# Kernel optimization log

Measured on AMD Instinct MI355X. Metric: run time of the kernel, lower is better.

## Reference

```python
import jax, jax.numpy as jnp
import numpy as np

HIDDEN = 2048
NUM_HEADS = 16
HEAD_DIM = HIDDEN // NUM_HEADS
SCALE = 1.0 / np.sqrt(HEAD_DIM).astype(np.float32)
BATCH, SEQ = 2, 2048


def setup_inputs() -> dict:
    key = jax.random.key(0)
    ks = jax.random.split(key, 9)
    std = 0.02
    inp = {
        'hidden_states': jax.random.normal(ks[0], (BATCH, SEQ, HIDDEN), jnp.float32),
        'attention_mask': jnp.zeros((BATCH, 1, 1, SEQ), jnp.float32),
        'Wq': jax.random.normal(ks[1], (HIDDEN, HIDDEN), jnp.float32) * std,
        'bq': jnp.zeros((HIDDEN,), jnp.float32),
        'Wk': jax.random.normal(ks[2], (HIDDEN, HIDDEN), jnp.float32) * std,
        'bk': jnp.zeros((HIDDEN,), jnp.float32),
        'Wv': jax.random.normal(ks[3], (HIDDEN, HIDDEN), jnp.float32) * std,
        'bv': jnp.zeros((HIDDEN,), jnp.float32),
        'Wo': jax.random.normal(ks[4], (HIDDEN, HIDDEN), jnp.float32) * std,
        'bo': jnp.zeros((HIDDEN,), jnp.float32),
    }
    return inp


def _split_heads(x):
    b, s, _ = x.shape
    return x.reshape(b, s, NUM_HEADS, HEAD_DIM).transpose(0, 2, 1, 3)  # [b,h,s,d]


def reference(hidden_states, attention_mask, Wq, bq, Wk, bk, Wv, bv, Wo, bo):
    # Linear layers (torch convention: y = x @ W.T + b)
    q = _split_heads(hidden_states @ Wq.T + bq)
    k = _split_heads(hidden_states @ Wk.T + bk)
    v = _split_heads(hidden_states @ Wv.T + bv)
    scores = jnp.einsum('bhqd,bhkd->bhqk', q, k) * SCALE
    scores = scores + attention_mask
    weights = jax.nn.softmax(scores, axis=-1)  # dropout is identity in eval
    ctx = jnp.einsum('bhqk,bhkd->bhqd', weights, v)
    b, h, s, d = ctx.shape
    ctx = ctx.transpose(0, 2, 1, 3).reshape(b, s, HIDDEN)
    return ctx @ Wo.T + bo
```

## Files before the change

kernel.cpp:

```cpp
#include <hip/hip_runtime.h>

typedef __bf16 bf16_t;
typedef bf16_t bf16x8 __attribute__((ext_vector_type(8)));
typedef float f32x4 __attribute__((ext_vector_type(4)));

#define HIDDEN 2048
#define SEQ 2048
#define BATCH 2
#define NHEADS 16
#define HDIM 128
#define MTOT (BATCH*SEQ)
#define SCALE 0.088388347648318447f
#define C1EXP2 0.12753102158508967f
#define LOG2E  1.4426950408889634f

__device__ __forceinline__ float dev_exp2(float x) { return __builtin_amdgcn_exp2f(x); }

typedef __attribute__((address_space(1))) const void gvoid_t;
typedef __attribute__((address_space(3))) void svoid_t;
__device__ __forceinline__ void async_copy16(const bf16_t* g, bf16_t* l) {
  __builtin_amdgcn_global_load_lds((gvoid_t*)g, (svoid_t*)l, 16, 0, 0);
}

__global__ void cvt_all(const float* __restrict__ x,  const float* __restrict__ wq,
                        const float* __restrict__ wk, const float* __restrict__ wv,
                        const float* __restrict__ wo,
                        bf16_t* __restrict__ xb, bf16_t* __restrict__ wqkb,
                        bf16_t* __restrict__ wvb, bf16_t* __restrict__ wob) {
  const size_t HH = (size_t)HIDDEN * HIDDEN;
  const float* src; bf16_t* dst;
  switch (blockIdx.y) {
    case 0:  src = x;        dst = xb;        break;
    case 1:  src = x + HH;   dst = xb + HH;   break;
    case 2:  src = wq;       dst = wqkb;      break;
    case 3:  src = wk;       dst = wqkb + HH; break;
    case 4:  src = wv;       dst = wvb;       break;
    default: src = wo;       dst = wob;       break;
  }
  int i = blockIdx.x * 256 + threadIdx.x;
  float4 v = reinterpret_cast<const float4*>(src)[i];
  union { bf16_t h[4]; uint2 u; } t;
  t.h[0] = (bf16_t)v.x; t.h[1] = (bf16_t)v.y; t.h[2] = (bf16_t)v.z; t.h[3] = (bf16_t)v.w;
  reinterpret_cast<uint2*>(dst)[i] = t.u;
}

__global__ void pack_bias2(const float* __restrict__ a, const float* __restrict__ b2,
                           float* __restrict__ out) {
  int i = blockIdx.x * 256 + threadIdx.x;
  out[i] = (i < HIDDEN) ? a[i] : b2[i - HIDDEN];
}

template<bool OUT_BF16, bool ROW_BIAS>
__global__ __launch_bounds__(256, 3)
void gemm_bt(const bf16_t* __restrict__ A, const bf16_t* __restrict__ Bt,
             const float* __restrict__ bias, void* __restrict__ Yv,
             int M, int N, int K, int ldY) {
  __shared__ __align__(16) bf16_t As[128 * 32];
  __shared__ __align__(16) bf16_t Bs[128 * 32];
  const int tid  = threadIdx.x;
  const int lane = tid & 63;
  const int wv   = tid >> 6;
  const int wr   = wv >> 1, wc = wv & 1;
  const int lr   = lane & 15, quad = lane >> 4;
  const int n0   = blockIdx.x * 128;
  const int m0   = blockIdx.y * 128;

  f32x4 acc[4][4] = {};

  const int srow = wv * 16 + (lane >> 2);
  const int scol = (lane & 3) * 8;
  const bf16_t* gA = A  + (size_t)(m0 + srow) * K + scol;
  const bf16_t* gB = Bt + (size_t)(n0 + srow) * K + scol;
  bf16_t* lA = &As[wv * 16 * 32];
  bf16_t* lB = &Bs[wv * 16 * 32];
  const size_t step64 = (size_t)64 * K;

  for (int kt = 0; kt < K; kt += 32) {
    __syncthreads();
    async_copy16(gA,          lA);
    async_copy16(gA + step64, lA + 64 * 32);
    async_copy16(gB,          lB);
    async_copy16(gB + step64, lB + 64 * 32);
    gA += 32; gB += 32;
    __syncthreads();
    bf16x8 af[4], bfr[4];
#pragma unroll
    for (int mi = 0; mi < 4; ++mi)
      af[mi] = *(const bf16x8*)&As[(wr * 64 + mi * 16 + lr) * 32 + quad * 8];
#pragma unroll
    for (int ni = 0; ni < 4; ++ni)
      bfr[ni] = *(const bf16x8*)&Bs[(wc * 64 + ni * 16 + lr) * 32 + quad * 8];
#pragma unroll
    for (int mi = 0; mi < 4; ++mi)
#pragma unroll
      for (int ni = 0; ni < 4; ++ni)
        acc[mi][ni] = __builtin_amdgcn_mfma_f32_16x16x32_bf16(af[mi], bfr[ni], acc[mi][ni], 0, 0, 0);
  }

  float bcol[4];
  if (!ROW_BIAS) {
#pragma unroll
    for (int ni = 0; ni < 4; ++ni) bcol[ni] = bias[n0 + wc * 64 + ni * 16 + lr];
  }
#pragma unroll
  for (int mi = 0; mi < 4; ++mi) {
#pragma unroll
    for (int r = 0; r < 4; ++r) {
      int row = m0 + wr * 64 + mi * 16 + quad * 4 + r;
      float brow = ROW_BIAS ? bias[row] : 0.0f;
      size_t base = (size_t)row * ldY + n0 + wc * 64;
#pragma unroll
      for (int ni = 0; ni < 4; ++ni) {
        float y = acc[mi][ni][r] + (ROW_BIAS ? brow : bcol[ni]);
        int col = ni * 16 + lr;
        if (OUT_BF16) ((bf16_t*)Yv)[base + col] = (bf16_t)y;
        else          ((float*)Yv)[base + col]  = y;
      }
    }
  }
}

#define BQ 128
#define BKV 64
#define LDQK 4096

__global__ __launch_bounds__(256, 2)
void attn_kernel(const bf16_t* __restrict__ QK, const bf16_t* __restrict__ Vt,
                 const float* __restrict__ mask, bf16_t* __restrict__ O) {
  __shared__ __align__(16) bf16_t Ks[2][BKV * 128];
  __shared__ __align__(16) bf16_t Vs[HDIM * BKV];
  __shared__ __align__(16) bf16_t Ps[BQ * BKV];
  __shared__ __align__(16) float  Msk[SEQ];

  const int tid  = threadIdx.x;
  const int lane = tid & 63;
  const int wv   = tid >> 6;
  const int lr   = lane & 15, quad = lane >> 4;
  const int q0   = blockIdx.x * BQ;
  const int bh   = blockIdx.y;
  const int b    = bh >> 4, h = bh & 15;

  const bf16_t* Qg = QK + (size_t)(b * SEQ + q0) * LDQK + h * HDIM;
  const bf16_t* Kg = QK + (size_t)(b * SEQ) * LDQK + HIDDEN + h * HDIM;
  const bf16_t* Vg = Vt + (size_t)(h * HDIM) * MTOT + b * SEQ;
  const float*  mb = mask + b * SEQ;

  bf16x8 qf[2][4];
#pragma unroll
  for (int mi = 0; mi < 2; ++mi)
#pragma unroll
    for (int dk = 0; dk < 4; ++dk)
      qf[mi][dk] = *(const bf16x8*)(Qg + (size_t)(wv * 32 + mi * 16 + lr) * LDQK + dk * 32 + quad * 8);

  for (int i = tid; i < SEQ / 4; i += 256) {
    float4 mv = reinterpret_cast<const float4*>(mb)[i];
    Msk[i * 4 + 0] = mv.x * LOG2E;
    Msk[i * 4 + 1] = mv.y * LOG2E;
    Msk[i * 4 + 2] = mv.z * LOG2E;
    Msk[i * 4 + 3] = mv.w * LOG2E;
  }

  const int kcs = lane & 15;
  const int vcs = lane & 7;
  const bf16_t* kgp[4]; const bf16_t* vgp[4];
  int lKo[4], lVo[4];
#pragma unroll
  for (int i = 0; i < 4; ++i) {
    int kr = wv * 16 + i * 4 + (lane >> 4);
    kgp[i] = Kg + (size_t)kr * LDQK + ((kcs ^ (kr & 15)) * 8);
    lKo[i] = (wv * 16 + i * 4) * 128;
    int vr = wv * 32 + i * 8 + (lane >> 3);
    vgp[i] = Vg + (size_t)vr * MTOT + ((vcs ^ (vr & 7)) * 8);
    lVo[i] = (wv * 32 + i * 8) * 64;
  }

  asm volatile("s_waitcnt vmcnt(0)" ::: "memory");
#pragma unroll
  for (int i = 0; i < 4; ++i) async_copy16(kgp[i], &Ks[0][lKo[i]]);
  asm volatile("s_waitcnt lgkmcnt(0)" ::: "memory");
  __builtin_amdgcn_s_barrier();

  float l_st[2][4] = {};
  f32x4 oacc[2][8] = {};

  for (int kt = 0; kt < SEQ; kt += BKV) {
    const int cur = (kt >> 6) & 1;
    const bf16_t* Kc = &Ks[cur][0];

    asm volatile("s_waitcnt lgkmcnt(0)" ::: "memory");
    __builtin_amdgcn_s_barrier();
#pragma unroll
    for (int i = 0; i < 4; ++i) async_copy16(vgp[i] + kt, &Vs[lVo[i]]);
    if (kt + BKV < SEQ) {
#pragma unroll
      for (int i = 0; i < 4; ++i)
        async_copy16(kgp[i] + (size_t)(kt + BKV) * LDQK, &Ks[cur ^ 1][lKo[i]]);
      asm volatile("s_waitcnt vmcnt(8)" ::: "memory");
    } else {
      asm volatile("s_waitcnt vmcnt(4)" ::: "memory");
    }
    __builtin_amdgcn_s_barrier();
    __builtin_amdgcn_sched_barrier(0);

    float mk[4];
#pragma unroll
    for (int ni = 0; ni < 4; ++ni) mk[ni] = Msk[kt + ni * 16 + lr];

    f32x4 sacc[2][4] = {};
#pragma unroll
    for (int dk = 0; dk < 4; ++dk) {
      bf16x8 kf[4];
#pragma unroll
      for (int ni = 0; ni < 4; ++ni)
        kf[ni] = *(const bf16x8*)&Kc[(ni * 16 + lr) * 128 + (((dk * 4 + quad) ^ lr) * 8)];
#pragma unroll
      for (int mi = 0; mi < 2; ++mi)
#pragma unroll
        for (int ni = 0; ni < 4; ++ni)
          sacc[mi][ni] = __builtin_amdgcn_mfma_f32_16x16x32_bf16(qf[mi][dk], kf[ni], sacc[mi][ni], 0, 0, 0);
    }

#pragma unroll
    for (int mi = 0; mi < 2; ++mi) {
#pragma unroll
      for (int r = 0; r < 4; ++r) {
        float p0 = dev_exp2(fmaf(sacc[mi][0][r], C1EXP2, mk[0]));
        float p1 = dev_exp2(fmaf(sacc[mi][1][r], C1EXP2, mk[1]));
        float p2 = dev_exp2(fmaf(sacc[mi][2][r], C1EXP2, mk[2]));
        float p3 = dev_exp2(fmaf(sacc[mi][3][r], C1EXP2, mk[3]));
        int pr = wv * 32 + mi * 16 + quad * 4 + r;
        int key = pr & 7;
        Ps[pr * BKV + (((0 + (lr >> 3)) ^ key) * 8) + (lr & 7)] = (bf16_t)p0;
        Ps[pr * BKV + (((2 + (lr >> 3)) ^ key) * 8) + (lr & 7)] = (bf16_t)p1;
        Ps[pr * BKV + (((4 + (lr >> 3)) ^ key) * 8) + (lr & 7)] = (bf16_t)p2;
        Ps[pr * BKV + (((6 + (lr >> 3)) ^ key) * 8) + (lr & 7)] = (bf16_t)p3;
        l_st[mi][r] += (p0 + p1) + (p2 + p3);
      }
    }

    if (kt + BKV < SEQ) {
      asm volatile("s_waitcnt vmcnt(4)" ::: "memory");
    } else {
      asm volatile("s_waitcnt vmcnt(0)" ::: "memory");
    }
    __builtin_amdgcn_s_barrier();
    __builtin_amdgcn_sched_barrier(0);

#pragma unroll
    for (int ki = 0; ki < 2; ++ki) {
      bf16x8 pf[2];
#pragma unroll
      for (int mi = 0; mi < 2; ++mi)
        pf[mi] = *(const bf16x8*)&Ps[(wv * 32 + mi * 16 + lr) * BKV + (((ki * 4 + quad) ^ (lr & 7)) * 8)];
#pragma unroll
      for (int di = 0; di < 8; ++di) {
        bf16x8 vf = *(const bf16x8*)&Vs[(di * 16 + lr) * BKV + (((ki * 4 + quad) ^ (lr & 7)) * 8)];
#pragma unroll
        for (int mi = 0; mi < 2; ++mi)
          oacc[mi][di] = __builtin_amdgcn_mfma_f32_16x16x32_bf16(pf[mi], vf, oacc[mi][di], 0, 0, 0);
      }
    }
  }

  bf16_t* Ob = O + (size_t)(b * SEQ + q0) * HIDDEN + h * HDIM;
#pragma unroll
  for (int mi = 0; mi < 2; ++mi) {
#pragma unroll
    for (int r = 0; r < 4; ++r) {
      float s = l_st[mi][r];
      s += __shfl_xor(s, 1);
      s += __shfl_xor(s, 2);
      s += __shfl_xor(s, 4);
      s += __shfl_xor(s, 8);
      float inv = 1.0f / s;
      size_t rowoff = (size_t)(wv * 32 + mi * 16 + quad * 4 + r) * HIDDEN;
#pragma unroll
      for (int di = 0; di < 8; ++di)
        Ob[rowoff + di * 16 + lr] = (bf16_t)(oacc[mi][di][r] * inv);
    }
  }
}

extern "C" void kernel_launch(void* const* d_in, const int* in_sizes, int n_in,
                              void* d_out, int out_size, void* d_ws, size_t ws_size,
                              hipStream_t stream) {
  const float* x   = (const float*)d_in[0];
  const float* msk = (const float*)d_in[1];
  const float* Wq  = (const float*)d_in[2];
  const float* bq  = (const float*)d_in[3];
  const float* Wk  = (const float*)d_in[4];
  const float* bk  = (const float*)d_in[5];
  const float* Wv  = (const float*)d_in[6];
  const float* bv  = (const float*)d_in[7];
  const float* Wo  = (const float*)d_in[8];
  const float* bo  = (const float*)d_in[9];
  float* out = (float*)d_out;

  bf16_t* Xb   = (bf16_t*)d_ws;
  bf16_t* Wqkb = Xb   + (size_t)MTOT * HIDDEN;
  bf16_t* Wvb  = Wqkb + (size_t)2 * HIDDEN * HIDDEN;
  bf16_t* Wob  = Wvb  + (size_t)HIDDEN * HIDDEN;
  bf16_t* QKo  = Wob  + (size_t)HIDDEN * HIDDEN;
  bf16_t* Vto  = QKo  + (size_t)MTOT * 2 * HIDDEN;
  float*  bqk  = (float*)(Vto + (size_t)HIDDEN * MTOT);
  bf16_t* Cb   = Xb;

  cvt_all<<<dim3(HIDDEN * HIDDEN / 4 / 256, 6), 256, 0, stream>>>(
      x, Wq, Wk, Wv, Wo, Xb, Wqkb, Wvb, Wob);
  pack_bias2<<<2 * HIDDEN / 256, 256, 0, stream>>>(bq, bk, bqk);

  gemm_bt<true, false><<<dim3(32, 32), 256, 0, stream>>>(Xb, Wqkb, bqk, QKo,
                                                         MTOT, 2 * HIDDEN, HIDDEN, 2 * HIDDEN);
  gemm_bt<true, true><<<dim3(32, 16), 256, 0, stream>>>(Wvb, Xb, bv, Vto,
                                                        HIDDEN, MTOT, HIDDEN, MTOT);
  attn_kernel<<<dim3(SEQ / BQ, BATCH * NHEADS), 256, 0, stream>>>(QKo, Vto, msk, Cb);
  gemm_bt<false, false><<<dim3(16, 32), 256, 0, stream>>>(Cb, Wob, bo, out,
                                                          MTOT, HIDDEN, HIDDEN, HIDDEN);
}
```

Measured before the change: 421.5 us.

## Add 256x256-tile 8-wave GEMM kernel for fused QK projection

Replaces the 128x128-tile generic GEMM for the Q/K projection with a dedicated 256x256-tile kernel using 512 threads. It double-buffers global-to-LDS loads with XOR-swizzled LDS layout, splits each k-step into four quarter MFMA phases with priority hints, and swizzles workgroup order for L2 locality. The larger tile raises arithmetic intensity per loaded byte, at the cost of 128KB of LDS per block and fewer blocks (256) for the device's CUs.

Measured after the change: 414.6 us. No clear change (-1.6%).

```diff
diff --git a/kernel.cpp b/kernel.cpp
--- a/kernel.cpp
+++ b/kernel.cpp
@@ -120,6 +120,114 @@
   }
 }
 
+#define QKK 2048
+#define STAGE256(buf, ktoff) do {                                              \
+  _Pragma("unroll") for (int i_ = 0; i_ < 4; ++i_)                             \
+    async_copy16(gA + (ktoff) + (size_t)(i_ * 8) * QKK,                        \
+                 &As[buf][(wv * 32 + i_ * 8) * 64]);                           \
+  _Pragma("unroll") for (int i_ = 0; i_ < 4; ++i_)                             \
+    async_copy16(gB + (ktoff) + (size_t)(i_ * 8) * QKK,                        \
+                 &Bs[buf][(wv * 32 + i_ * 8) * 64]);                           \
+} while (0)
+#define DS_A256(mh) do {                                                       \
+  _Pragma("unroll") for (int mi_ = 0; mi_ < 4; ++mi_)                          \
+    _Pragma("unroll") for (int kk_ = 0; kk_ < 2; ++kk_)                        \
+      af[mi_][kk_] = *(const bf16x8*)&As[p][(wr * 128 + ((mh)*4 + mi_) * 16 + lr) * 64 \
+                                           + (((kk_ * 4 + quad) ^ (lr & 7)) * 8)];     \
+} while (0)
+#define DS_B256(nh) do {                                                       \
+  _Pragma("unroll") for (int ni_ = 0; ni_ < 2; ++ni_)                          \
+    _Pragma("unroll") for (int kk_ = 0; kk_ < 2; ++kk_)                        \
+      bfq[ni_][kk_] = *(const bf16x8*)&Bs[p][(wc * 64 + ((nh)*2 + ni_) * 16 + lr) * 64 \
+                                            + (((kk_ * 4 + quad) ^ (lr & 7)) * 8)];    \
+} while (0)
+#define MFMA_Q256(mh, nh) do {                                                 \
+  __builtin_amdgcn_s_setprio(1);                                               \
+  _Pragma("unroll") for (int mi_ = 0; mi_ < 4; ++mi_)                          \
+    _Pragma("unroll") for (int ni_ = 0; ni_ < 2; ++ni_) {                      \
+      acc[(mh)*4 + mi_][(nh)*2 + ni_] = __builtin_amdgcn_mfma_f32_16x16x32_bf16( \
+          af[mi_][0], bfq[ni_][0], acc[(mh)*4 + mi_][(nh)*2 + ni_], 0, 0, 0);  \
+      acc[(mh)*4 + mi_][(nh)*2 + ni_] = __builtin_amdgcn_mfma_f32_16x16x32_bf16( \
+          af[mi_][1], bfq[ni_][1], acc[(mh)*4 + mi_][(nh)*2 + ni_], 0, 0, 0);  \
+    }                                                                          \
+  __builtin_amdgcn_s_setprio(0);                                               \
+} while (0)
+
+__global__ __launch_bounds__(512, 2)
+void gemm256_bt(const bf16_t* __restrict__ A, const bf16_t* __restrict__ Bt,
+                const float* __restrict__ bias, bf16_t* __restrict__ Y) {
+  __shared__ __align__(16) bf16_t As[2][256 * 64];
+  __shared__ __align__(16) bf16_t Bs[2][256 * 64];
+  const int tid  = threadIdx.x;
+  const int lane = tid & 63;
+  const int wv   = tid >> 6;
+  const int wr   = wv >> 2, wc = wv & 3;
+  const int lr   = lane & 15, quad = lane >> 4;
+
+  const int wg  = blockIdx.x;
+  const int swz = (wg & 7) * 32 + (wg >> 3);
+  const int m0  = (swz >> 4) * 256;
+  const int n0  = (swz & 15) * 256;
+
+  f32x4 acc[8][4] = {};
+
+  const int sub = lane >> 3;
+  const int ch  = (lane & 7) ^ sub;
+  const bf16_t* gA = A  + (size_t)(m0 + wv * 32 + sub) * QKK + ch * 8;
+  const bf16_t* gB = Bt + (size_t)(n0 + wv * 32 + sub) * QKK + ch * 8;
+
+  STAGE256(0, 0);
+  asm volatile("s_waitcnt vmcnt(0)" ::: "memory");
+  __builtin_amdgcn_s_barrier();
+
+  bf16x8 af[4][2], bfq[2][2];
+
+  for (int t = 0; t < QKK / 64; ++t) {
+    const int p   = t & 1;
+    const int ktb = t * 64;
+
+    if (t + 1 < QKK / 64) STAGE256(p ^ 1, ktb + 64);
+    DS_A256(0); DS_B256(0);
+    asm volatile("s_waitcnt lgkmcnt(0)" ::: "memory");
+    __builtin_amdgcn_sched_barrier(0);
+    MFMA_Q256(0, 0);
+    __builtin_amdgcn_s_barrier();
+
+    DS_B256(1);
+    asm volatile("s_waitcnt lgkmcnt(0)" ::: "memory");
+    __builtin_amdgcn_sched_barrier(0);
+    MFMA_Q256(0, 1);
+    __builtin_amdgcn_s_barrier();
+
+    DS_A256(1);
+    asm volatile("s_waitcnt lgkmcnt(0)" ::: "memory");
+    __builtin_amdgcn_sched_barrier(0);
+    MFMA_Q256(1, 1);
+    __builtin_amdgcn_s_barrier();
+
+    DS_B256(0);
+    asm volatile("s_waitcnt vmcnt(0) lgkmcnt(0)" ::: "memory");
+    __builtin_amdgcn_sched_barrier(0);
+    MFMA_Q256(1, 0);
+    __builtin_amdgcn_s_barrier();
+  }
+
+  float bcol[4];
+#pragma unroll
+  for (int ni = 0; ni < 4; ++ni) bcol[ni] = bias[n0 + wc * 64 + ni * 16 + lr];
+#pragma unroll
+  for (int fm = 0; fm < 8; ++fm) {
+#pragma unroll
+    for (int r = 0; r < 4; ++r) {
+      size_t row  = (size_t)(m0 + wr * 128 + fm * 16 + quad * 4 + r);
+      size_t base = row * 4096 + n0 + wc * 64;
+#pragma unroll
+      for (int ni = 0; ni < 4; ++ni)
+        Y[base + ni * 16 + lr] = (bf16_t)(acc[fm][ni][r] + bcol[ni]);
+    }
+  }
+}
+
 #define BQ 128
 #define BKV 64
 #define LDQK 4096
@@ -309,8 +417,7 @@
       x, Wq, Wk, Wv, Wo, Xb, Wqkb, Wvb, Wob);
   pack_bias2<<<2 * HIDDEN / 256, 256, 0, stream>>>(bq, bk, bqk);
 
-  gemm_bt<true, false><<<dim3(32, 32), 256, 0, stream>>>(Xb, Wqkb, bqk, QKo,
-                                                         MTOT, 2 * HIDDEN, HIDDEN, 2 * HIDDEN);
+  gemm256_bt<<<256, 512, 0, stream>>>(Xb, Wqkb, bqk, QKo);
   gemm_bt<true, true><<<dim3(32, 16), 256, 0, stream>>>(Wvb, Xb, bv, Vto,
                                                         HIDDEN, MTOT, HIDDEN, MTOT);
   attn_kernel<<<dim3(SEQ / BQ, BATCH * NHEADS), 256, 0, stream>>>(QKo, Vto, msk, Cb);
```

## Replace GEMM with 256x256-tile 8-wave double-buffered pipelined kernel

Applied to the files above, without the earlier changes.

Replaces the simple 128x128, single-buffered GEMM with a 512-thread kernel that computes 256x256 tiles using K-steps of 64. LDS is double-buffered with XOR-swizzled layout to avoid bank conflicts, and global-to-LDS async copies are interleaved with four MFMA phases separated by barriers. It also adds workgroup index swizzling for L2 locality and s_setprio around MFMA bursts. The aim is to hide global memory latency and raise MFMA utilization. The cost is more LDS and register pressure, and fewer workgroups, which means lower occupancy.

New measurement: 421.5 us. About the same (+0.0%).

```diff
diff --git a/kernel.cpp b/kernel.cpp
--- a/kernel.cpp
+++ b/kernel.cpp
@@ -50,69 +50,121 @@
   out[i] = (i < HIDDEN) ? a[i] : b2[i - HIDDEN];
 }
 
+#define RD_A(dst, buf, mh) do {                                                \
+  _Pragma("unroll") for (int mi_ = 0; mi_ < 4; ++mi_)                          \
+    _Pragma("unroll") for (int kk_ = 0; kk_ < 2; ++kk_)                        \
+      dst[mi_][kk_] = *(const bf16x8*)&As[buf][mh][(wr * 64 + mi_ * 16 + lr) * 64 \
+                         + (((kk_ * 4 + quad) ^ (lr & 7)) * 8)];               \
+} while (0)
+#define RD_B(dst, buf, nh) do {                                                \
+  _Pragma("unroll") for (int ni_ = 0; ni_ < 2; ++ni_)                          \
+    _Pragma("unroll") for (int kk_ = 0; kk_ < 2; ++kk_)                        \
+      dst[ni_][kk_] = *(const bf16x8*)&Bs[buf][nh][(wc * 32 + ni_ * 16 + lr) * 64 \
+                         + (((kk_ * 4 + quad) ^ (lr & 7)) * 8)];               \
+} while (0)
+#define MMQ(mh, nh, afr, bfr) do {                                             \
+  __builtin_amdgcn_s_setprio(1);                                               \
+  _Pragma("unroll") for (int mi_ = 0; mi_ < 4; ++mi_)                          \
+    _Pragma("unroll") for (int ni_ = 0; ni_ < 2; ++ni_) {                      \
+      acc[(mh)*4 + mi_][(nh)*2 + ni_] = __builtin_amdgcn_mfma_f32_16x16x32_bf16( \
+          afr[mi_][0], bfr[ni_][0], acc[(mh)*4 + mi_][(nh)*2 + ni_], 0, 0, 0); \
+      acc[(mh)*4 + mi_][(nh)*2 + ni_] = __builtin_amdgcn_mfma_f32_16x16x32_bf16( \
+          afr[mi_][1], bfr[ni_][1], acc[(mh)*4 + mi_][(nh)*2 + ni_], 0, 0, 0); \
+    }                                                                          \
+  __builtin_amdgcn_s_setprio(0);                                               \
+} while (0)
+#define STG(ptr, t64, ldsbase) do {                                            \
+  async_copy16((ptr) + (t64), (ldsbase));                                      \
+  async_copy16((ptr) + (size_t)8 * K + (t64), (ldsbase) + 8 * 64);             \
+} while (0)
+#define PHASE_SYNC do { __builtin_amdgcn_s_barrier();                          \
+  asm volatile("s_waitcnt lgkmcnt(0)" ::: "memory");                           \
+  __builtin_amdgcn_sched_barrier(0); } while (0)
+
 template<bool OUT_BF16, bool ROW_BIAS>
-__global__ __launch_bounds__(256, 3)
-void gemm_bt(const bf16_t* __restrict__ A, const bf16_t* __restrict__ Bt,
-             const float* __restrict__ bias, void* __restrict__ Yv,
-             int M, int N, int K, int ldY) {
-  __shared__ __align__(16) bf16_t As[128 * 32];
-  __shared__ __align__(16) bf16_t Bs[128 * 32];
+__global__ __launch_bounds__(512)
+void gemm8p(const bf16_t* __restrict__ A, const bf16_t* __restrict__ Bt,
+            const float* __restrict__ bias, void* __restrict__ Yv,
+            int K, int ldY, int nbt) {
+  __shared__ __align__(16) bf16_t As[2][2][128 * 64];
+  __shared__ __align__(16) bf16_t Bs[2][2][128 * 64];
   const int tid  = threadIdx.x;
   const int lane = tid & 63;
   const int wv   = tid >> 6;
-  const int wr   = wv >> 1, wc = wv & 1;
+  const int wr   = wv >> 2, wc = wv & 3;
   const int lr   = lane & 15, quad = lane >> 4;
-  const int n0   = blockIdx.x * 128;
-  const int m0   = blockIdx.y * 128;
-
-  f32x4 acc[4][4] = {};
-
-  const int srow = wv * 16 + (lane >> 2);
-  const int scol = (lane & 3) * 8;
-  const bf16_t* gA = A  + (size_t)(m0 + srow) * K + scol;
-  const bf16_t* gB = Bt + (size_t)(n0 + srow) * K + scol;
-  bf16_t* lA = &As[wv * 16 * 32];
-  bf16_t* lB = &Bs[wv * 16 * 32];
-  const size_t step64 = (size_t)64 * K;
-
-  for (int kt = 0; kt < K; kt += 32) {
-    __syncthreads();
-    async_copy16(gA,          lA);
-    async_copy16(gA + step64, lA + 64 * 32);
-    async_copy16(gB,          lB);
-    async_copy16(gB + step64, lB + 64 * 32);
-    gA += 32; gB += 32;
-    __syncthreads();
-    bf16x8 af[4], bfr[4];
-#pragma unroll
-    for (int mi = 0; mi < 4; ++mi)
-      af[mi] = *(const bf16x8*)&As[(wr * 64 + mi * 16 + lr) * 32 + quad * 8];
-#pragma unroll
-    for (int ni = 0; ni < 4; ++ni)
-      bfr[ni] = *(const bf16x8*)&Bs[(wc * 64 + ni * 16 + lr) * 32 + quad * 8];
-#pragma unroll
-    for (int mi = 0; mi < 4; ++mi)
-#pragma unroll
-      for (int ni = 0; ni < 4; ++ni)
-        acc[mi][ni] = __builtin_amdgcn_mfma_f32_16x16x32_bf16(af[mi], bfr[ni], acc[mi][ni], 0, 0, 0);
-  }
-
-  float bcol[4];
+
+  const int wg  = blockIdx.x;
+  const int cpx = gridDim.x >> 3;
+  const int swz = (wg & 7) * cpx + (wg >> 3);
+  const int m0  = (swz / nbt) * 256;
+  const int n0  = (swz % nbt) * 256;
+
+  f32x4 acc[8][4] = {};
+
+  const int sub = lane >> 3, chv = (lane & 7) ^ sub;
+  const int rih = wv * 16 + sub;
+  const bf16_t* pA0 = A  + (size_t)(m0 +       rih) * K + chv * 8;
+  const bf16_t* pA1 = A  + (size_t)(m0 + 128 + rih) * K + chv * 8;
+  const bf16_t* pB0 = Bt + (size_t)(n0 +       rih) * K + chv * 8;
+  const bf16_t* pB1 = Bt + (size_t)(n0 + 128 + rih) * K + chv * 8;
+  const int lwo = wv * 16 * 64;
+  const int nt  = K >> 6;
+
+  STG(pB0, (size_t)0,  &Bs[0][0][lwo]);
+  STG(pA0, (size_t)0,  &As[0][0][lwo]);
+  STG(pA1, (size_t)0,  &As[0][1][lwo]);
+  STG(pB1, (size_t)0,  &Bs[0][1][lwo]);
+  STG(pB0, (size_t)64, &Bs[1][0][lwo]);
+  STG(pA0, (size_t)64, &As[1][0][lwo]);
+  asm volatile("s_waitcnt vmcnt(2)" ::: "memory");
+  __builtin_amdgcn_s_barrier();
+
+  bf16x8 af0[4][2], af1[4][2], bf0[2][2], bf1[2][2];
+
+  for (int t = 0; t < nt; ++t) {
+    const int p = t & 1;
+    const size_t tk = (size_t)t * 64;
+
+    RD_A(af0, p, 0); RD_B(bf0, p, 0);
+    if (t + 1 < nt) STG(pA1, tk + 64, &As[p ^ 1][1][lwo]);
+    PHASE_SYNC; MMQ(0, 0, af0, bf0); __builtin_amdgcn_s_barrier();
+
+    RD_A(af1, p, 1);
+    if (t + 1 < nt) STG(pB1, tk + 64, &Bs[p ^ 1][1][lwo]);
+    PHASE_SYNC; MMQ(1, 0, af1, bf0); __builtin_amdgcn_s_barrier();
+
+    RD_B(bf1, p, 1);
+    if (t + 2 < nt) STG(pB0, tk + 128, &Bs[p][0][lwo]);
+    PHASE_SYNC; MMQ(0, 1, af0, bf1); __builtin_amdgcn_s_barrier();
+
+    if (t + 2 < nt) {
+      STG(pA0, tk + 128, &As[p][0][lwo]);
+      asm volatile("s_waitcnt vmcnt(4)" ::: "memory");
+    } else {
+      asm volatile("s_waitcnt vmcnt(0)" ::: "memory");
+    }
+    PHASE_SYNC; MMQ(1, 1, af1, bf1); __builtin_amdgcn_s_barrier();
+  }
+
+  float bc[4];
   if (!ROW_BIAS) {
 #pragma unroll
-    for (int ni = 0; ni < 4; ++ni) bcol[ni] = bias[n0 + wc * 64 + ni * 16 + lr];
-  }
-#pragma unroll
-  for (int mi = 0; mi < 4; ++mi) {
+    for (int fn = 0; fn < 4; ++fn)
+      bc[fn] = bias[n0 + (fn >> 1) * 128 + wc * 32 + (fn & 1) * 16 + lr];
+  }
+#pragma unroll
+  for (int fm = 0; fm < 8; ++fm) {
+    const int rowb = m0 + (fm >> 2) * 128 + wr * 64 + (fm & 3) * 16 + quad * 4;
 #pragma unroll
     for (int r = 0; r < 4; ++r) {
-      int row = m0 + wr * 64 + mi * 16 + quad * 4 + r;
-      float brow = ROW_BIAS ? bias[row] : 0.0f;
-      size_t base = (size_t)row * ldY + n0 + wc * 64;
-#pragma unroll
-      for (int ni = 0; ni < 4; ++ni) {
-        float y = acc[mi][ni][r] + (ROW_BIAS ? brow : bcol[ni]);
-        int col = ni * 16 + lr;
+      const int row = rowb + r;
+      const float brow = ROW_BIAS ? bias[row] : 0.0f;
+      const size_t base = (size_t)row * ldY;
+#pragma unroll
+      for (int fn = 0; fn < 4; ++fn) {
+        const int col = n0 + (fn >> 1) * 128 + wc * 32 + (fn & 1) * 16 + lr;
+        float y = acc[fm][fn][r] + (ROW_BIAS ? brow : bc[fn]);
         if (OUT_BF16) ((bf16_t*)Yv)[base + col] = (bf16_t)y;
         else          ((float*)Yv)[base + col]  = y;
       }
@@ -309,11 +361,8 @@
       x, Wq, Wk, Wv, Wo, Xb, Wqkb, Wvb, Wob);
   pack_bias2<<<2 * HIDDEN / 256, 256, 0, stream>>>(bq, bk, bqk);
 
-  gemm_bt<true, false><<<dim3(32, 32), 256, 0, stream>>>(Xb, Wqkb, bqk, QKo,
-                                                         MTOT, 2 * HIDDEN, HIDDEN, 2 * HIDDEN);
-  gemm_bt<true, true><<<dim3(32, 16), 256, 0, stream>>>(Wvb, Xb, bv, Vto,
-                                                        HIDDEN, MTOT, HIDDEN, MTOT);
+  gemm8p<true, false><<<256, 512, 0, stream>>>(Xb, Wqkb, bqk, QKo, HIDDEN, 4096, 16);
+  gemm8p<true, true><<<128, 512, 0, stream>>>(Wvb, Xb, bv, Vto, HIDDEN, 4096, 16);
   attn_kernel<<<dim3(SEQ / BQ, BATCH * NHEADS), 256, 0, stream>>>(QKo, Vto, msk, Cb);
-  gemm_bt<false, false><<<dim3(16, 32), 256, 0, stream>>>(Cb, Wob, bo, out,
-                                                          MTOT, HIDDEN, HIDDEN, HIDDEN);
-}
+  gemm8p<false, false><<<128, 512, 0, stream>>>(Cb, Wob, bo, out, HIDDEN, 2048, 8);
+}
```
